# Kernel optimization log

Measured on AMD Instinct MI355X. Metric: run time of the kernel, lower is better.

## Reference

```python
import jax, jax.numpy as jnp
import numpy as np

B, S, D, H = 256, 100, 512, 8
HD = D // H  # head_dim = 64


def setup_inputs() -> dict:
    key = jax.random.key(0)
    ks = jax.random.split(key, 12)
    scale = 1.0 / np.sqrt(D)
    return {
        "x": jax.random.normal(ks[0], (B, S, D), dtype=jnp.float32),
        "pos_emb": jax.random.normal(ks[1], (1, 100, D), dtype=jnp.float32),
        "temporal_decay": jnp.float32(0.95),
        # torch nn.Linear weights are [out, in]; applied as x @ W.T + b
        "Wq": jax.random.normal(ks[2], (D, D), dtype=jnp.float32) * scale,
        "bq": jax.random.normal(ks[3], (D,), dtype=jnp.float32) * scale,
        "Wk": jax.random.normal(ks[4], (D, D), dtype=jnp.float32) * scale,
        "bk": jax.random.normal(ks[5], (D,), dtype=jnp.float32) * scale,
        "Wv": jax.random.normal(ks[6], (D, D), dtype=jnp.float32) * scale,
        "bv": jax.random.normal(ks[7], (D,), dtype=jnp.float32) * scale,
        "Wo": jax.random.normal(ks[8], (D, D), dtype=jnp.float32) * scale,
        "bo": jax.random.normal(ks[9], (D,), dtype=jnp.float32) * scale,
    }


def reference(x, pos_emb, temporal_decay, Wq, bq, Wk, bk, Wv, bv, Wo, bo):
    b, s, d = x.shape
    xp = x + pos_emb[:, :s, :]  # add position embeddings to Q/K input only

    def heads(t):  # [b,s,d] -> [b,H,s,HD]
        return t.reshape(b, s, H, HD).transpose(0, 2, 1, 3)

    q = heads(xp @ Wq.T + bq)
    k = heads(xp @ Wk.T + bk)
    v = heads(x @ Wv.T + bv)  # V uses x WITHOUT positions (per source)

    scores = jnp.einsum("bhqd,bhkd->bhqk", q, k) / np.sqrt(HD)
    # decay over KEY positions: decay^(s-1), ..., decay^1, decay^0
    exponents = jnp.arange(s - 1, -1, -1, dtype=jnp.float32)
    decay = temporal_decay ** exponents  # [s]
    scores = scores * decay[None, None, None, :]

    attn = jax.nn.softmax(scores, axis=-1)  # dropout is identity in eval
    ctx = jnp.einsum("bhqk,bhkd->bhqd", attn, v)
    ctx = ctx.transpose(0, 2, 1, 3).reshape(b, s, d)
    out = ctx @ Wo.T + bo
    return out, attn
```

## Files before the change

### kernel.cpp

```cpp
#include <hip/hip_runtime.h>
#include <hip/hip_bf16.h>
#include <cmath>

#define B_   256
#define S_   100
#define D_   512
#define H_   8
#define HD_  64
#define BS_  (B_ * S_)
#define OUT_ELEMS  (BS_ * D_)
#define ATTN_ELEMS (B_ * H_ * S_ * S_)
#define DD_  (D_ * D_)

typedef __bf16 bf16x8 __attribute__((ext_vector_type(8)));
typedef float  f32x4  __attribute__((ext_vector_type(4)));

__device__ __forceinline__ void gload16(const void* g, void* l) {
    __builtin_amdgcn_global_load_lds(
        (const __attribute__((address_space(1))) void*)g,
        (__attribute__((address_space(3))) void*)l, 16, 0, 0);
}

__device__ __forceinline__ void stage_tile(const __hip_bfloat16* __restrict__ src,
                                           char* ldsTile, int t) {
    #pragma unroll
    for (int i = 0; i < 4; ++i) {
        const int ci  = i * 256 + t;
        const int row = ci >> 3;
        const int sc  = (ci & 7) ^ (row & 7);
        gload16(src + (size_t)row * D_ + sc * 8,
                ldsTile + ((i * 256 + (t & 192)) << 4));
    }
}

__device__ __forceinline__ void compute_tile(const char* ldsA, const char* ldsB,
                                             int lane, int wr, int wc,
                                             f32x4 acc[4][4]) {
    const int frow = lane & 15;
    const int fk   = lane >> 4;
    #pragma unroll
    for (int kk = 0; kk < 2; ++kk) {
        const int ch = kk * 4 + fk;
        bf16x8 af[4], bfr[4];
        #pragma unroll
        for (int m = 0; m < 4; ++m) {
            const int row = wr + m * 16 + frow;
            af[m] = *(const bf16x8*)(ldsA + row * 128 + ((ch ^ (row & 7)) << 4));
        }
        #pragma unroll
        for (int n = 0; n < 4; ++n) {
            const int row = wc + n * 16 + frow;
            bfr[n] = *(const bf16x8*)(ldsB + row * 128 + ((ch ^ (row & 7)) << 4));
        }
        #pragma unroll
        for (int m = 0; m < 4; ++m)
            #pragma unroll
            for (int n = 0; n < 4; ++n)
                acc[m][n] = __builtin_amdgcn_mfma_f32_16x16x32_bf16(
                    af[m], bfr[n], acc[m][n], 0, 0, 0);
    }
}

__global__ __launch_bounds__(256) void qkv_gemm(
    const __hip_bfloat16* __restrict__ apos,
    const __hip_bfloat16* __restrict__ wall,
    const float* __restrict__ bq, const float* __restrict__ bk,
    const float* __restrict__ bv, const float* __restrict__ pv,
    __hip_bfloat16* __restrict__ qkv)
{
    const int z = blockIdx.z;
    const __hip_bfloat16* W    = wall + (size_t)z * DD_;
    const float*          bias = (z == 0) ? bq : (z == 1) ? bk : bv;
    __hip_bfloat16*       out  = qkv + (size_t)z * OUT_ELEMS;

    __shared__ __align__(16) char lds[2][2][16384];
    const int t    = threadIdx.x;
    const int r0   = blockIdx.x * 128, c0 = blockIdx.y * 128;
    const int lane = t & 63, wid = t >> 6;
    const int wr   = (wid >> 1) << 6, wc = (wid & 1) << 6;

    f32x4 acc[4][4] = {};

    const __hip_bfloat16* Ab = apos + (size_t)r0 * D_;
    const __hip_bfloat16* Bb = W    + (size_t)c0 * D_;

    stage_tile(Ab, lds[0][0], t);
    stage_tile(Bb, lds[0][1], t);
    asm volatile("s_waitcnt vmcnt(0)" ::: "memory");
    __syncthreads();

    int cur = 0;
    for (int kt = 1; kt < 8; ++kt) {
        stage_tile(Ab + kt * 64, lds[cur ^ 1][0], t);
        stage_tile(Bb + kt * 64, lds[cur ^ 1][1], t);
        compute_tile(lds[cur][0], lds[cur][1], lane, wr, wc, acc);
        asm volatile("s_waitcnt vmcnt(0)" ::: "memory");
        __syncthreads();
        cur ^= 1;
    }
    compute_tile(lds[cur][0], lds[cur][1], lane, wr, wc, acc);

    const int fcol = lane & 15, fq = lane >> 4;
    #pragma unroll
    for (int n = 0; n < 4; ++n) {
        const int c  = c0 + wc + n * 16 + fcol;
        const float bi = bias[c];
        const int h = c >> 6, hd = c & 63;
        #pragma unroll
        for (int m = 0; m < 4; ++m) {
            const int rbase = r0 + wr + m * 16 + fq * 4;
            #pragma unroll
            for (int r = 0; r < 4; ++r) {
                const int rowg = rbase + r;
                const int b = rowg / S_;
                const int s = rowg - b * S_;
                float v = acc[m][n][r] + bi;
                if (z == 2) v -= pv[s * D_ + c];
                out[(((size_t)b * H_ + h) * S_ + s) * HD_ + hd] = __float2bfloat16(v);
            }
        }
    }
}

__global__ __launch_bounds__(256) void outproj_gemm(
    const __hip_bfloat16* __restrict__ ctx,
    const __hip_bfloat16* __restrict__ Wo,
    const float* __restrict__ bo,
    float* __restrict__ out)
{
    __shared__ __align__(16) char lds[2][2][16384];
    const int t    = threadIdx.x;
    const int r0   = blockIdx.x * 128, c0 = blockIdx.y * 128;
    const int lane = t & 63, wid = t >> 6;
    const int wr   = (wid >> 1) << 6, wc = (wid & 1) << 6;

    f32x4 acc[4][4] = {};

    const __hip_bfloat16* Ab = ctx + (size_t)r0 * D_;
    const __hip_bfloat16* Bb = Wo  + (size_t)c0 * D_;

    stage_tile(Ab, lds[0][0], t);
    stage_tile(Bb, lds[0][1], t);
    asm volatile("s_waitcnt vmcnt(0)" ::: "memory");
    __syncthreads();

    int cur = 0;
    for (int kt = 1; kt < 8; ++kt) {
        stage_tile(Ab + kt * 64, lds[cur ^ 1][0], t);
        stage_tile(Bb + kt * 64, lds[cur ^ 1][1], t);
        compute_tile(lds[cur][0], lds[cur][1], lane, wr, wc, acc);
        asm volatile("s_waitcnt vmcnt(0)" ::: "memory");
        __syncthreads();
        cur ^= 1;
    }
    compute_tile(lds[cur][0], lds[cur][1], lane, wr, wc, acc);

    const int fcol = lane & 15, fq = lane >> 4;
    #pragma unroll
    for (int n = 0; n < 4; ++n) {
        const int c  = c0 + wc + n * 16 + fcol;
        const float bi = bo[c];
        #pragma unroll
        for (int m = 0; m < 4; ++m) {
            const int rbase = r0 + wr + m * 16 + fq * 4;
            #pragma unroll
            for (int r = 0; r < 4; ++r) {
                const int rowg = rbase + r;
                out[(size_t)rowg * D_ + c] = acc[m][n][r] + bi;
            }
        }
    }
}

__global__ __launch_bounds__(256) void attn_mfma(
    const __hip_bfloat16* __restrict__ qkv,
    float* __restrict__ attn_out,
    __hip_bfloat16* __restrict__ ctx,
    const float* __restrict__ td_ptr)
{
    __shared__ __align__(16) __hip_bfloat16 Vt[2][64][136];
    __shared__ __align__(16) __hip_bfloat16 Pl[4][16][136];
    __shared__ float dec[128];

    const int t    = threadIdx.x;
    const int lane = t & 63, wid = t >> 6;
    const int c    = lane & 15, g4 = lane >> 4;
    const int bh0  = blockIdx.x * 2;

    if (t < 128)
        dec[t] = (t < S_) ? 0.125f * powf(td_ptr[0], (float)(S_ - 1 - t)) : 0.f;

    {
        const int h = wid >> 1;
        const int k = ((wid & 1) << 6) + lane;
        if (k < S_) {
            const __hip_bfloat16* vr = qkv + 2 * (size_t)OUT_ELEMS
                                     + (size_t)(bh0 + h) * (S_ * HD_)
                                     + (size_t)k * HD_;
            #pragma unroll
            for (int j8 = 0; j8 < 8; ++j8) {
                uint4 u = *(const uint4*)(vr + j8 * 8);
                const __hip_bfloat16* e = (const __hip_bfloat16*)&u;
                #pragma unroll
                for (int ee = 0; ee < 8; ++ee)
                    Vt[h][j8 * 8 + ee][k] = e[ee];
            }
        }
        for (int idx = t; idx < 2 * 64 * 9; idx += 256) {
            const int hh  = idx / 576;
            const int rem = idx - hh * 576;
            const int d   = rem / 9, c8 = rem - d * 9;
            *(double*)((char*)&Vt[hh][d][100] + c8 * 8) = 0.0;
        }
    }
    *(double*)&Pl[wid][c][112 + 4 * g4] = 0.0;
    __syncthreads();

    float decr[7][4];
    #pragma unroll
    for (int kt = 0; kt < 7; ++kt)
        #pragma unroll
        for (int r = 0; r < 4; ++r)
            decr[kt][r] = dec[16 * kt + 4 * g4 + r];

    for (int item = wid; item < 14; item += 4) {
        const int hh = item / 7;
        const int qt = item - hh * 7;
        const int bh = bh0 + hh;
        const __hip_bfloat16* Qb = qkv + (size_t)bh * (S_ * HD_);
        const __hip_bfloat16* Kb = qkv + (size_t)OUT_ELEMS + (size_t)bh * (S_ * HD_);

        const bf16x8 qf0 = *(const bf16x8*)(Qb + (16 * qt + c) * HD_ + 8 * g4);
        const bf16x8 qf1 = *(const bf16x8*)(Qb + (16 * qt + c) * HD_ + 32 + 8 * g4);

        f32x4 s[7] = {};
        #pragma unroll
        for (int kt = 0; kt < 7; ++kt) {
            const bf16x8 kf0 = *(const bf16x8*)(Kb + (16 * kt + c) * HD_ + 8 * g4);
            const bf16x8 kf1 = *(const bf16x8*)(Kb + (16 * kt + c) * HD_ + 32 + 8 * g4);
            s[kt] = __builtin_amdgcn_mfma_f32_16x16x32_bf16(kf0, qf0, s[kt], 0, 0, 0);
            s[kt] = __builtin_amdgcn_mfma_f32_16x16x32_bf16(kf1, qf1, s[kt], 0, 0, 0);
        }

        float m = -3.0e38f;
        #pragma unroll
        for (int kt = 0; kt < 7; ++kt)
            #pragma unroll
            for (int r = 0; r < 4; ++r) {
                float v = s[kt][r] * decr[kt][r];
                if (kt == 6 && (4 * g4 + r) >= 4) v = -3.0e38f;
                s[kt][r] = v;
                m = fmaxf(m, v);
            }
        m = fmaxf(m, __shfl_xor(m, 16, 64));
        m = fmaxf(m, __shfl_xor(m, 32, 64));

        float sum = 0.f;
        #pragma unroll
        for (int kt = 0; kt < 7; ++kt)
            #pragma unroll
            for (int r = 0; r < 4; ++r) {
                const float p = __expf(s[kt][r] - m);
                s[kt][r] = p;
                sum += p;
            }
        sum += __shfl_xor(sum, 16, 64);
        sum += __shfl_xor(sum, 32, 64);
        const float rs = 1.0f / sum;

        const int qg = 16 * qt + c;
        float* arow = attn_out + (size_t)bh * (S_ * S_) + (size_t)qg * S_;
        #pragma unroll
        for (int kt = 0; kt < 7; ++kt) {
            const float a0 = s[kt][0] * rs, a1 = s[kt][1] * rs;
            const float a2 = s[kt][2] * rs, a3 = s[kt][3] * rs;
            if (qg < S_ && (kt < 6 || g4 == 0))
                *(float4*)(arow + 16 * kt + 4 * g4) = make_float4(a0, a1, a2, a3);
            __align__(8) __hip_bfloat16 pb[4];
            pb[0] = __float2bfloat16(a0); pb[1] = __float2bfloat16(a1);
            pb[2] = __float2bfloat16(a2); pb[3] = __float2bfloat16(a3);
            *(double*)&Pl[wid][c][16 * kt + 4 * g4] = *(double*)pb;
        }

        f32x4 o[4] = {};
        #pragma unroll
        for (int kk = 0; kk < 4; ++kk) {
            const bf16x8 pf = *(const bf16x8*)&Pl[wid][c][32 * kk + 8 * g4];
            #pragma unroll
            for (int dt = 0; dt < 4; ++dt) {
                const bf16x8 vf = *(const bf16x8*)&Vt[hh][16 * dt + c][32 * kk + 8 * g4];
                o[dt] = __builtin_amdgcn_mfma_f32_16x16x32_bf16(pf, vf, o[dt], 0, 0, 0);
            }
        }

        const int b = bh >> 3, h = bh & 7;
        #pragma unroll
        for (int r = 0; r < 4; ++r) {
            const int q = 16 * qt + 4 * g4 + r;
            if (q < S_) {
                __hip_bfloat16* crow = ctx + (size_t)(b * S_ + q) * D_ + h * HD_ + c;
                #pragma unroll
                for (int dt = 0; dt < 4; ++dt)
                    crow[16 * dt] = __float2bfloat16(o[dt][r]);
            }
        }
    }
}

__global__ __launch_bounds__(256) void conv_apos_kernel(
    const float* __restrict__ x, const float* __restrict__ pos,
    __hip_bfloat16* __restrict__ apos)
{
    const int i8   = (blockIdx.x * 256 + threadIdx.x) * 8;
    const int row  = i8 >> 9;
    const int prow = row % S_;
    const int pcol = i8 & 511;
    const float4* xv = (const float4*)(x + i8);
    const float4* pp = (const float4*)(pos + (size_t)prow * D_ + pcol);
    float4 a0 = xv[0], a1 = xv[1], p0 = pp[0], p1 = pp[1];
    __align__(16) __hip_bfloat16 o[8];
    o[0] = __float2bfloat16(a0.x + p0.x); o[1] = __float2bfloat16(a0.y + p0.y);
    o[2] = __float2bfloat16(a0.z + p0.z); o[3] = __float2bfloat16(a0.w + p0.w);
    o[4] = __float2bfloat16(a1.x + p1.x); o[5] = __float2bfloat16(a1.y + p1.y);
    o[6] = __float2bfloat16(a1.z + p1.z); o[7] = __float2bfloat16(a1.w + p1.w);
    *(uint4*)(apos + i8) = *(const uint4*)o;
}

__global__ __launch_bounds__(256) void conv_w_kernel(
    const float* __restrict__ Wq, const float* __restrict__ Wk,
    const float* __restrict__ Wv, const float* __restrict__ Wo,
    __hip_bfloat16* __restrict__ wall)
{
    const int z = blockIdx.y;
    const float* src = (z == 0) ? Wq : (z == 1) ? Wk : (z == 2) ? Wv : Wo;
    __hip_bfloat16* dst = wall + (size_t)z * DD_;
    const int i8 = (blockIdx.x * 256 + threadIdx.x) * 8;
    const float4* sv = (const float4*)(src + i8);
    float4 a0 = sv[0], a1 = sv[1];
    __align__(16) __hip_bfloat16 o[8];
    o[0] = __float2bfloat16(a0.x); o[1] = __float2bfloat16(a0.y);
    o[2] = __float2bfloat16(a0.z); o[3] = __float2bfloat16(a0.w);
    o[4] = __float2bfloat16(a1.x); o[5] = __float2bfloat16(a1.y);
    o[6] = __float2bfloat16(a1.z); o[7] = __float2bfloat16(a1.w);
    *(uint4*)(dst + i8) = *(const uint4*)o;
}

__global__ __launch_bounds__(256) void posv_kernel(
    const float* __restrict__ pos, const float* __restrict__ Wv,
    float* __restrict__ pvout)
{
    const int idx = blockIdx.x * 256 + threadIdx.x;
    const int s = idx >> 9, c = idx & 511;
    const float4* pr = (const float4*)(pos + (size_t)s * D_);
    const float4* wr = (const float4*)(Wv + (size_t)c * D_);
    float a = 0.f;
    #pragma unroll 4
    for (int k = 0; k < D_ / 4; ++k) {
        float4 p = pr[k], w = wr[k];
        a = fmaf(p.x, w.x, a); a = fmaf(p.y, w.y, a);
        a = fmaf(p.z, w.z, a); a = fmaf(p.w, w.w, a);
    }
    pvout[idx] = a;
}

extern "C" void kernel_launch(void* const* d_in, const int* in_sizes, int n_in,
                              void* d_out, int out_size, void* d_ws, size_t ws_size,
                              hipStream_t stream) {
    (void)in_sizes; (void)n_in; (void)out_size; (void)ws_size;
    const float* x   = (const float*)d_in[0];
    const float* pos = (const float*)d_in[1];
    const float* td  = (const float*)d_in[2];
    const float* Wq  = (const float*)d_in[3];
    const float* bq  = (const float*)d_in[4];
    const float* Wk  = (const float*)d_in[5];
    const float* bk  = (const float*)d_in[6];
    const float* Wv  = (const float*)d_in[7];
    const float* bv  = (const float*)d_in[8];
    const float* Wo  = (const float*)d_in[9];
    const float* bo  = (const float*)d_in[10];

    float* out  = (float*)d_out;
    float* attn = out + (size_t)OUT_ELEMS;

    char* ws = (char*)d_ws;
    __hip_bfloat16* apos = (__hip_bfloat16*)ws;
    __hip_bfloat16* qkv  = (__hip_bfloat16*)(ws + 26214400);
    __hip_bfloat16* ctx  = (__hip_bfloat16*)(ws + 104857600);
    __hip_bfloat16* wall = (__hip_bfloat16*)(ws + 131072000);
    float*          pvb  = (float*)(ws + 133169152);

    conv_apos_kernel<<<OUT_ELEMS / 8 / 256, 256, 0, stream>>>(x, pos, apos);
    conv_w_kernel<<<dim3(DD_ / 8 / 256, 4), 256, 0, stream>>>(Wq, Wk, Wv, Wo, wall);
    posv_kernel<<<(S_ * D_) / 256, 256, 0, stream>>>(pos, Wv, pvb);

    qkv_gemm<<<dim3(BS_ / 128, D_ / 128, 3), 256, 0, stream>>>(
        apos, wall, bq, bk, bv, pvb, qkv);
    attn_mfma<<<B_ * H_ / 2, 256, 0, stream>>>(qkv, attn, ctx, td);
    outproj_gemm<<<dim3(BS_ / 128, D_ / 128), 256, 0, stream>>>(
        ctx, wall + 3 * (size_t)DD_, bo, out);
}
```

Before: 216.3 us.

## Load weight fragments directly from global memory instead of staging through LDS

Both GEMM kernels now stage only the activation tile into LDS. Each wave reads its weight (B) MFMA fragments straight from global memory into registers, which halves the LDS footprint and drops half of the LDS traffic. MFMA sections are also wrapped in s_setprio to raise wave priority during the math. The cost is that the weight loads become synchronous global loads on the compute path, waited on by the vmcnt(0) barrier. Each weight row is also reread by the two waves that share a column slice, and that reuse now has to come from cache.

```diff
diff --git a/kernel.cpp b/kernel.cpp
--- a/kernel.cpp
+++ b/kernel.cpp
@@ -33,31 +33,34 @@
     }
 }
 
-__device__ __forceinline__ void compute_tile(const char* ldsA, const char* ldsB,
-                                             int lane, int wr, int wc,
-                                             f32x4 acc[4][4]) {
+__device__ __forceinline__ void compute_tile_bg(
+    const char* ldsA, const __hip_bfloat16* __restrict__ Wt,
+    int lane, int wr, f32x4 acc[4][4])
+{
     const int frow = lane & 15;
     const int fk   = lane >> 4;
     #pragma unroll
     for (int kk = 0; kk < 2; ++kk) {
         const int ch = kk * 4 + fk;
-        bf16x8 af[4], bfr[4];
+        bf16x8 bfr[4];
+        #pragma unroll
+        for (int n = 0; n < 4; ++n)
+            bfr[n] = *(const bf16x8*)(Wt + (size_t)(n * 16 + frow) * D_
+                                      + kk * 32 + fk * 8);
+        bf16x8 af[4];
         #pragma unroll
         for (int m = 0; m < 4; ++m) {
             const int row = wr + m * 16 + frow;
             af[m] = *(const bf16x8*)(ldsA + row * 128 + ((ch ^ (row & 7)) << 4));
         }
-        #pragma unroll
-        for (int n = 0; n < 4; ++n) {
-            const int row = wc + n * 16 + frow;
-            bfr[n] = *(const bf16x8*)(ldsB + row * 128 + ((ch ^ (row & 7)) << 4));
-        }
+        __builtin_amdgcn_s_setprio(1);
         #pragma unroll
         for (int m = 0; m < 4; ++m)
             #pragma unroll
             for (int n = 0; n < 4; ++n)
                 acc[m][n] = __builtin_amdgcn_mfma_f32_16x16x32_bf16(
                     af[m], bfr[n], acc[m][n], 0, 0, 0);
+        __builtin_amdgcn_s_setprio(0);
     }
 }
 
@@ -73,7 +76,7 @@
     const float*          bias = (z == 0) ? bq : (z == 1) ? bk : bv;
     __hip_bfloat16*       out  = qkv + (size_t)z * OUT_ELEMS;
 
-    __shared__ __align__(16) char lds[2][2][16384];
+    __shared__ __align__(16) char lds[2][16384];
     const int t    = threadIdx.x;
     const int r0   = blockIdx.x * 128, c0 = blockIdx.y * 128;
     const int lane = t & 63, wid = t >> 6;
@@ -82,23 +85,21 @@
     f32x4 acc[4][4] = {};
 
     const __hip_bfloat16* Ab = apos + (size_t)r0 * D_;
-    const __hip_bfloat16* Bb = W    + (size_t)c0 * D_;
-
-    stage_tile(Ab, lds[0][0], t);
-    stage_tile(Bb, lds[0][1], t);
+    const __hip_bfloat16* Wb = W + (size_t)(c0 + wc) * D_;
+
+    stage_tile(Ab, lds[0], t);
     asm volatile("s_waitcnt vmcnt(0)" ::: "memory");
     __syncthreads();
 
     int cur = 0;
     for (int kt = 1; kt < 8; ++kt) {
-        stage_tile(Ab + kt * 64, lds[cur ^ 1][0], t);
-        stage_tile(Bb + kt * 64, lds[cur ^ 1][1], t);
-        compute_tile(lds[cur][0], lds[cur][1], lane, wr, wc, acc);
+        stage_tile(Ab + kt * 64, lds[cur ^ 1], t);
+        compute_tile_bg(lds[cur], Wb + (kt - 1) * 64, lane, wr, acc);
         asm volatile("s_waitcnt vmcnt(0)" ::: "memory");
         __syncthreads();
         cur ^= 1;
     }
-    compute_tile(lds[cur][0], lds[cur][1], lane, wr, wc, acc);
+    compute_tile_bg(lds[cur], Wb + 7 * 64, lane, wr, acc);
 
     const int fcol = lane & 15, fq = lane >> 4;
     #pragma unroll
@@ -128,7 +129,7 @@
     const float* __restrict__ bo,
     float* __restrict__ out)
 {
-    __shared__ __align__(16) char lds[2][2][16384];
+    __shared__ __align__(16) char lds[2][16384];
     const int t    = threadIdx.x;
     const int r0   = blockIdx.x * 128, c0 = blockIdx.y * 128;
     const int lane = t & 63, wid = t >> 6;
@@ -137,23 +138,21 @@
     f32x4 acc[4][4] = {};
 
     const __hip_bfloat16* Ab = ctx + (size_t)r0 * D_;
-    const __hip_bfloat16* Bb = Wo  + (size_t)c0 * D_;
-
-    stage_tile(Ab, lds[0][0], t);
-    stage_tile(Bb, lds[0][1], t);
+    const __hip_bfloat16* Wb = Wo + (size_t)(c0 + wc) * D_;
+
+    stage_tile(Ab, lds[0], t);
     asm volatile("s_waitcnt vmcnt(0)" ::: "memory");
     __syncthreads();
 
     int cur = 0;
     for (int kt = 1; kt < 8; ++kt) {
-        stage_tile(Ab + kt * 64, lds[cur ^ 1][0], t);
-        stage_tile(Bb + kt * 64, lds[cur ^ 1][1], t);
-        compute_tile(lds[cur][0], lds[cur][1], lane, wr, wc, acc);
+        stage_tile(Ab + kt * 64, lds[cur ^ 1], t);
+        compute_tile_bg(lds[cur], Wb + (kt - 1) * 64, lane, wr, acc);
         asm volatile("s_waitcnt vmcnt(0)" ::: "memory");
         __syncthreads();
         cur ^= 1;
     }
-    compute_tile(lds[cur][0], lds[cur][1], lane, wr, wc, acc);
+    compute_tile_bg(lds[cur], Wb + 7 * 64, lane, wr, acc);
 
     const int fcol = lane & 15, fq = lane >> 4;
     #pragma unroll
```

After: 258.3 us. 1.19x slower.

## Fuse Q/K/V GEMMs into one block sharing the staged A tile

Applied to the files above, without the earlier changes.

The QKV projection now runs as a single kernel with 512 threads per block. Each block stages one A tile and all three weight tiles, so the activation tile is loaded once instead of three times, and each wave computes a 64x32 output tile for each of Q, K and V. It also raises wave priority around the MFMA bursts with s_setprio. LDS use per block grows to 128KB with double buffering, which limits occupancy to one block per CU and reduces the grid by a factor of three.

```diff
diff --git a/kernel.cpp b/kernel.cpp
--- a/kernel.cpp
+++ b/kernel.cpp
@@ -33,6 +33,18 @@
     }
 }
 
+__device__ __forceinline__ void stage_tile512(const __hip_bfloat16* __restrict__ src,
+                                              char* ldsTile, int t) {
+    #pragma unroll
+    for (int i = 0; i < 2; ++i) {
+        const int ci  = i * 512 + t;
+        const int row = ci >> 3;
+        const int sc  = (ci & 7) ^ (row & 7);
+        gload16(src + (size_t)row * D_ + sc * 8,
+                ldsTile + ((i * 512 + (t & 448)) << 4));
+    }
+}
+
 __device__ __forceinline__ void compute_tile(const char* ldsA, const char* ldsB,
                                              int lane, int wr, int wc,
                                              f32x4 acc[4][4]) {
@@ -52,71 +64,116 @@
             const int row = wc + n * 16 + frow;
             bfr[n] = *(const bf16x8*)(ldsB + row * 128 + ((ch ^ (row & 7)) << 4));
         }
+        __builtin_amdgcn_s_setprio(1);
         #pragma unroll
         for (int m = 0; m < 4; ++m)
             #pragma unroll
             for (int n = 0; n < 4; ++n)
                 acc[m][n] = __builtin_amdgcn_mfma_f32_16x16x32_bf16(
                     af[m], bfr[n], acc[m][n], 0, 0, 0);
-    }
-}
-
-__global__ __launch_bounds__(256) void qkv_gemm(
+        __builtin_amdgcn_s_setprio(0);
+    }
+}
+
+__device__ __forceinline__ void compute_fused(const char* buf, int lane,
+                                              int wr, int wc,
+                                              f32x4 acc[3][4][2]) {
+    const int frow = lane & 15;
+    const int fk   = lane >> 4;
+    #pragma unroll
+    for (int kk = 0; kk < 2; ++kk) {
+        const int ch = kk * 4 + fk;
+        bf16x8 af[4];
+        #pragma unroll
+        for (int m = 0; m < 4; ++m) {
+            const int row = wr + m * 16 + frow;
+            af[m] = *(const bf16x8*)(buf + row * 128 + ((ch ^ (row & 7)) << 4));
+        }
+        bf16x8 bfr[3][2];
+        #pragma unroll
+        for (int z = 0; z < 3; ++z)
+            #pragma unroll
+            for (int n = 0; n < 2; ++n) {
+                const int row = wc + n * 16 + frow;
+                bfr[z][n] = *(const bf16x8*)(buf + 16384 + z * 16384
+                                             + row * 128 + ((ch ^ (row & 7)) << 4));
+            }
+        __builtin_amdgcn_s_setprio(1);
+        #pragma unroll
+        for (int z = 0; z < 3; ++z)
+            #pragma unroll
+            for (int m = 0; m < 4; ++m)
+                #pragma unroll
+                for (int n = 0; n < 2; ++n)
+                    acc[z][m][n] = __builtin_amdgcn_mfma_f32_16x16x32_bf16(
+                        af[m], bfr[z][n], acc[z][m][n], 0, 0, 0);
+        __builtin_amdgcn_s_setprio(0);
+    }
+}
+
+__global__ __launch_bounds__(512) void qkv_gemm(
     const __hip_bfloat16* __restrict__ apos,
     const __hip_bfloat16* __restrict__ wall,
     const float* __restrict__ bq, const float* __restrict__ bk,
     const float* __restrict__ bv, const float* __restrict__ pv,
     __hip_bfloat16* __restrict__ qkv)
 {
-    const int z = blockIdx.z;
-    const __hip_bfloat16* W    = wall + (size_t)z * DD_;
-    const float*          bias = (z == 0) ? bq : (z == 1) ? bk : bv;
-    __hip_bfloat16*       out  = qkv + (size_t)z * OUT_ELEMS;
-
-    __shared__ __align__(16) char lds[2][2][16384];
+    __shared__ __align__(16) char lds[2][65536];
     const int t    = threadIdx.x;
     const int r0   = blockIdx.x * 128, c0 = blockIdx.y * 128;
     const int lane = t & 63, wid = t >> 6;
-    const int wr   = (wid >> 1) << 6, wc = (wid & 1) << 6;
-
-    f32x4 acc[4][4] = {};
+    const int wr   = (wid >> 2) << 6;
+    const int wc   = (wid & 3) << 5;
+
+    f32x4 acc[3][4][2] = {};
 
     const __hip_bfloat16* Ab = apos + (size_t)r0 * D_;
-    const __hip_bfloat16* Bb = W    + (size_t)c0 * D_;
-
-    stage_tile(Ab, lds[0][0], t);
-    stage_tile(Bb, lds[0][1], t);
+
+    stage_tile512(Ab, lds[0], t);
+    #pragma unroll
+    for (int z = 0; z < 3; ++z)
+        stage_tile512(wall + (size_t)z * DD_ + (size_t)c0 * D_,
+                      lds[0] + 16384 + z * 16384, t);
     asm volatile("s_waitcnt vmcnt(0)" ::: "memory");
     __syncthreads();
 
     int cur = 0;
     for (int kt = 1; kt < 8; ++kt) {
-        stage_tile(Ab + kt * 64, lds[cur ^ 1][0], t);
-        stage_tile(Bb + kt * 64, lds[cur ^ 1][1], t);
-        compute_tile(lds[cur][0], lds[cur][1], lane, wr, wc, acc);
+        stage_tile512(Ab + kt * 64, lds[cur ^ 1], t);
+        #pragma unroll
+        for (int z = 0; z < 3; ++z)
+            stage_tile512(wall + (size_t)z * DD_ + (size_t)c0 * D_ + kt * 64,
+                          lds[cur ^ 1] + 16384 + z * 16384, t);
+        compute_fused(lds[cur], lane, wr, wc, acc);
         asm volatile("s_waitcnt vmcnt(0)" ::: "memory");
         __syncthreads();
         cur ^= 1;
     }
-    compute_tile(lds[cur][0], lds[cur][1], lane, wr, wc, acc);
+    compute_fused(lds[cur], lane, wr, wc, acc);
 
     const int fcol = lane & 15, fq = lane >> 4;
     #pragma unroll
-    for (int n = 0; n < 4; ++n) {
-        const int c  = c0 + wc + n * 16 + fcol;
-        const float bi = bias[c];
-        const int h = c >> 6, hd = c & 63;
-        #pragma unroll
-        for (int m = 0; m < 4; ++m) {
-            const int rbase = r0 + wr + m * 16 + fq * 4;
-            #pragma unroll
-            for (int r = 0; r < 4; ++r) {
-                const int rowg = rbase + r;
-                const int b = rowg / S_;
-                const int s = rowg - b * S_;
-                float v = acc[m][n][r] + bi;
-                if (z == 2) v -= pv[s * D_ + c];
-                out[(((size_t)b * H_ + h) * S_ + s) * HD_ + hd] = __float2bfloat16(v);
+    for (int z = 0; z < 3; ++z) {
+        const float* bias = (z == 0) ? bq : (z == 1) ? bk : bv;
+        __hip_bfloat16* outz = qkv + (size_t)z * OUT_ELEMS;
+        #pragma unroll
+        for (int n = 0; n < 2; ++n) {
+            const int c  = c0 + wc + n * 16 + fcol;
+            const float bi = bias[c];
+            const int h = c >> 6, hd = c & 63;
+            #pragma unroll
+            for (int m = 0; m < 4; ++m) {
+                const int rbase = r0 + wr + m * 16 + fq * 4;
+                #pragma unroll
+                for (int r = 0; r < 4; ++r) {
+                    const int rowg = rbase + r;
+                    const int b = rowg / S_;
+                    const int s = rowg - b * S_;
+                    float v = acc[z][m][n][r] + bi;
+                    if (z == 2) v -= pv[s * D_ + c];
+                    outz[(((size_t)b * H_ + h) * S_ + s) * HD_ + hd] =
+                        __float2bfloat16(v);
+                }
             }
         }
     }
@@ -393,7 +450,7 @@
     conv_w_kernel<<<dim3(DD_ / 8 / 256, 4), 256, 0, stream>>>(Wq, Wk, Wv, Wo, wall);
     posv_kernel<<<(S_ * D_) / 256, 256, 0, stream>>>(pos, Wv, pvb);
 
-    qkv_gemm<<<dim3(BS_ / 128, D_ / 128, 3), 256, 0, stream>>>(
+    qkv_gemm<<<dim3(BS_ / 128, D_ / 128), 512, 0, stream>>>(
         apos, wall, bq, bk, bv, pvb, qkv);
     attn_mfma<<<B_ * H_ / 2, 256, 0, stream>>>(qkv, attn, ctx, td);
     outproj_gemm<<<dim3(BS_ / 128, D_ / 128), 256, 0, stream>>>(
```

Result: faster. 187.3 us (-13.4%).
